# Optimization experiments

Measured on AMD Instinct MI355X. Metric: run time of the kernel, lower is better.

## Reference

```python
import jax, jax.numpy as jnp
import numpy as np

# Dimensions
T, B = 128, 512
NTOK, NINP, NHID = 512, 512, 600
NB, BS, TOPK = 6, 100, 4          # num_blocks, block_size = nhid//num_blocks, update_topk
H, DK, DV, ATT = 4, 64, 85, 340   # input-attention heads, key dim, value dim (H*DV == attention_out)
H2, DK2, DV2 = 4, 32, 32          # communication (step) attention dims


def setup_inputs() -> dict:
    key = jax.random.key(0)
    ks = jax.random.split(key, 16)
    def rn(k, shape, s=0.05):
        return (jax.random.normal(k, shape) * s).astype(jnp.float32)
    return dict(
        input=jax.random.normal(ks[0], (T, B, NTOK), dtype=jnp.float32),
        h0=jnp.zeros((B, NHID), jnp.float32),
        masks=jnp.ones((T, B, 1), jnp.float32),
        enc_W=rn(ks[1], (NTOK, NINP)), enc_b=jnp.zeros((NINP,), jnp.float32),
        Wq_in=rn(ks[2], (BS, H * DK)), Wk_in=rn(ks[3], (NINP, H * DK)), Wv_in=rn(ks[4], (NINP, H * DV)),
        W_ih=rn(ks[5], (NB, ATT, 3 * BS)), W_hh=rn(ks[6], (NB, BS, 3 * BS)),
        b_ih=jnp.zeros((NB, 3 * BS), jnp.float32), b_hh=jnp.zeros((NB, 3 * BS), jnp.float32),
        Wq_c=rn(ks[7], (BS, H2 * DK2)), Wk_c=rn(ks[8], (BS, H2 * DK2)),
        Wv_c=rn(ks[9], (BS, H2 * DV2)), Wo_c=rn(ks[10], (H2 * DV2, BS)),
        dec_W=rn(ks[11], (NHID, NTOK)), dec_b=jnp.zeros((NTOK,), jnp.float32),
    )


def _rim_scan(emb, masks, h0, Wq_in, Wk_in, Wv_in, W_ih, W_hh, b_ih, b_hh,
              Wq_c, Wk_c, Wv_c, Wo_c):
    inv_sdk = 1.0 / np.sqrt(DK).astype(np.float32)
    inv_sdk2 = 1.0 / np.sqrt(DK2).astype(np.float32)

    def step(h, xm):
        xt, mt = xm                      # [B,NINP], [B,1]
        h = h * mt                       # episode-reset gating
        hb = h.reshape(B, NB, BS)
        # --- input attention over {real input, null} slots ---
        slots = jnp.stack([xt, jnp.zeros_like(xt)], axis=1)          # [B,2,NINP]
        k = (slots @ Wk_in).reshape(B, 2, H, DK)
        v = (slots @ Wv_in).reshape(B, 2, H, DV)
        q = (hb @ Wq_in).reshape(B, NB, H, DK)
        att = jax.nn.softmax(jnp.einsum('bnhd,bshd->bnhs', q, k) * inv_sdk, axis=-1)
        act = 1.0 - att[..., 1].mean(-1)                             # [B,NB] attention to real input
        kth = jax.lax.top_k(act, TOPK)[0][:, -1:]
        mask = (act >= kth).astype(h.dtype)                          # [B,NB] top-k block activation
        inp_use = jnp.einsum('bnhs,bshd->bnhd', att, v).reshape(B, NB, ATT)
        # --- block-diagonal GRU update ---
        gi = jnp.einsum('bnd,nde->bne', inp_use, W_ih) + b_ih
        gh = jnp.einsum('bnd,nde->bne', hb, W_hh) + b_hh
        gi_r, gi_z, gi_n = jnp.split(gi, 3, axis=-1)
        gh_r, gh_z, gh_n = jnp.split(gh, 3, axis=-1)
        r = jax.nn.sigmoid(gi_r + gh_r)
        z = jax.nn.sigmoid(gi_z + gh_z)
        n = jnp.tanh(gi_n + r * gh_n)
        hn = (1.0 - z) * n + z * hb
        # --- step (communication) attention across blocks, residual ---
        qc = (hn @ Wq_c).reshape(B, NB, H2, DK2)
        kc = (hn @ Wk_c).reshape(B, NB, H2, DK2)
        vc = (hn @ Wv_c).reshape(B, NB, H2, DV2)
        ac = jax.nn.softmax(jnp.einsum('bnhd,bmhd->bhnm', qc, kc) * inv_sdk2, axis=-1)
        co = jnp.einsum('bhnm,bmhd->bnhd', ac, vc).reshape(B, NB, H2 * DV2) @ Wo_c
        hc = hn + co
        # --- only top-k active blocks are updated ---
        m = mask[..., None]
        hf = (m * hc + (1.0 - m) * hb).reshape(B, NHID)
        return hf, (hf, mask)

    h_last, (hs, bmask) = jax.lax.scan(step, h0, (emb, masks))
    return hs, h_last, bmask


def reference(input, h0, masks, enc_W, enc_b, Wq_in, Wk_in, Wv_in,
              W_ih, W_hh, b_ih, b_hh, Wq_c, Wk_c, Wv_c, Wo_c, dec_W, dec_b):
    emb = input @ enc_W + enc_b                                      # encoder Linear [T,B,NINP]
    hs, h_last, bmask = _rim_scan(emb, masks, h0, Wq_in, Wk_in, Wv_in,
                                  W_ih, W_hh, b_ih, b_hh, Wq_c, Wk_c, Wv_c, Wo_c)
    dec = hs @ dec_W + dec_b                                         # decoder [T,B,NTOK]
    return dec
```

## Files before the change

kernel.cpp:

```cpp
#include <hip/hip_runtime.h>
#include <math.h>

#define T_STEPS 128
#define BATCH   512
#define NTOK    512
#define NINP    512
#define NHID    600
#define NBK     6
#define BS      100
#define HH      4
#define DK      64
#define DV      85
#define ATT     340
#define H2      4
#define DK2     32
#define DV2     32
#define G3      300
#define VN      340
#define KAPN    400
#define CN      740
#define CNP     768
#define UN2     1800
#define UN2P    1920
#define UK0     128
#define KV0     512
#define DECKP   640
#define SW      2

typedef __attribute__((ext_vector_type(8))) short short8;
typedef __attribute__((ext_vector_type(4))) short short4v;
typedef __attribute__((ext_vector_type(4))) float f32x4;

typedef __attribute__((address_space(1))) const unsigned int* g1ptr;
typedef __attribute__((address_space(3))) unsigned int* l3ptr;

__device__ __forceinline__ float sigf(float x) { return 1.f / (1.f + expf(-x)); }
__device__ __forceinline__ unsigned short f2b(float f) {
    unsigned u = __float_as_uint(f);
    unsigned r = (u + 0x7fffu + ((u >> 16) & 1u)) >> 16;
    return (unsigned short)r;
}
__device__ __forceinline__ float b2f(unsigned short u) {
    return __uint_as_float(((unsigned)u) << 16);
}
__device__ __forceinline__ void split3(float x, unsigned short& hi,
                                       unsigned short& mid, unsigned short& lo) {
    hi = f2b(x);
    float r1 = x - b2f(hi);
    mid = f2b(r1);
    lo = f2b(r1 - b2f(mid));
}

struct ZOff { int div; long s1; long s2; };
__device__ __forceinline__ long zoff(ZOff z, int bz) {
    return (long)(bz / z.div) * z.s1 + (long)(bz % z.div) * z.s2;
}

__device__ __forceinline__ void stage_tile(const unsigned short* __restrict__ gbase,
                                           long rowStride, int m0, int k0,
                                           unsigned short* lds, int tid)
{
    const int w = tid >> 6;
#pragma unroll
    for (int q = 0; q < 4; q++) {
        int idx = (q << 8) + tid;
        int r = idx >> 3, ce = (idx & 7) << 3;
        const unsigned short* g = gbase + (long)(m0 + r) * rowStride + k0 + ce;
        unsigned short* l = lds + q * 2048 + w * 512;
        __builtin_amdgcn_global_load_lds((g1ptr)(const void*)g, (l3ptr)(void*)l, 16, 0, 0);
    }
}
__device__ __forceinline__ void stage_tile64(const unsigned short* __restrict__ gbase,
                                             long rowStride, int m0, int k0,
                                             unsigned short* lds, int tid)
{
    const int w = tid >> 6;
#pragma unroll
    for (int q = 0; q < 2; q++) {
        int idx = (q << 8) + tid;
        int r = idx >> 3, ce = (idx & 7) << 3;
        const unsigned short* g = gbase + (long)(m0 + r) * rowStride + k0 + ce;
        unsigned short* l = lds + q * 2048 + w * 512;
        __builtin_amdgcn_global_load_lds((g1ptr)(const void*)g, (l3ptr)(void*)l, 16, 0, 0);
    }
}

__global__ __launch_bounds__(256) void gemm6(
    const unsigned short* __restrict__ A, long aZ, int aZdiv,
    const unsigned short* __restrict__ B, long bZ,
    float* __restrict__ C, long cZ, int ldc, int Nreal,
    const float* __restrict__ bias, int K0)
{
    const int bz = blockIdx.z;
    A += (long)(bz / aZdiv) * aZ;
    B += (long)bz * bZ;
    C += (long)bz * cZ;
    const int LDA = 3 * K0;
    const int m0 = blockIdx.y * 128, n0 = blockIdx.x * 128;
    __shared__ __align__(16) unsigned short As[128 * 64];
    __shared__ __align__(16) unsigned short Bs[128 * 64];
    const int tid = threadIdx.x;
    const int lane = tid & 63;
    const int wid = tid >> 6;
    const int wr = wid >> 1, wc = wid & 1;

    f32x4 acc[4][4];
#pragma unroll
    for (int m = 0; m < 4; m++)
#pragma unroll
        for (int n = 0; n < 4; n++)
#pragma unroll
            for (int v = 0; v < 4; v++) acc[m][n][v] = 0.f;

    const int segA[6] = {0, 0, 1, 0, 2, 1};
    const int segB[6] = {0, 1, 0, 2, 0, 1};
    for (int p = 0; p < 6; p++) {
        const unsigned short* Ap = A + segA[p] * K0;
        const unsigned short* Bp = B + segB[p] * K0;
        for (int k0 = 0; k0 < K0; k0 += 64) {
            __syncthreads();
            stage_tile(Ap, LDA, m0, k0, As, tid);
            stage_tile(Bp, LDA, n0, k0, Bs, tid);
            __syncthreads();
#pragma unroll
            for (int kk = 0; kk < 2; kk++) {
                short8 af[4], bfr[4];
#pragma unroll
                for (int m = 0; m < 4; m++)
                    af[m] = *(const short8*)&As[(wr * 64 + m * 16 + (lane & 15)) * 64 + kk * 32 + (lane >> 4) * 8];
#pragma unroll
                for (int n = 0; n < 4; n++)
                    bfr[n] = *(const short8*)&Bs[(wc * 64 + n * 16 + (lane & 15)) * 64 + kk * 32 + (lane >> 4) * 8];
#pragma unroll
                for (int m = 0; m < 4; m++)
#pragma unroll
                    for (int n = 0; n < 4; n++)
                        acc[m][n] = __builtin_amdgcn_mfma_f32_16x16x32_bf16(af[m], bfr[n], acc[m][n], 0, 0, 0);
            }
        }
    }
#pragma unroll
    for (int m = 0; m < 4; m++) {
        int rbase = m0 + wr * 64 + m * 16 + (lane >> 4) * 4;
#pragma unroll
        for (int n = 0; n < 4; n++) {
            int col = n0 + wc * 64 + n * 16 + (lane & 15);
            if (col < Nreal) {
                float bv = bias ? bias[col] : 0.f;
#pragma unroll
                for (int v = 0; v < 4; v++)
                    C[(long)(rbase + v) * ldc + col] = acc[m][n][v] + bv;
            }
        }
    }
}

__global__ __launch_bounds__(256) void gemm6_kv64(
    const unsigned short* __restrict__ A,
    const unsigned short* __restrict__ B,
    unsigned short* __restrict__ A_U,
    float* __restrict__ Kbuf,
    const float* __restrict__ bias, int K0, int MU)
{
    const int LDA = 3 * K0;
    const int m0 = blockIdx.y * 64, n0 = blockIdx.x * 128;
    __shared__ __align__(16) unsigned short As[64 * 64];
    __shared__ __align__(16) unsigned short Bs[128 * 64];
    const int tid = threadIdx.x;
    const int lane = tid & 63;
    const int w = tid >> 6;

    f32x4 acc[4][2];
#pragma unroll
    for (int m = 0; m < 4; m++)
#pragma unroll
        for (int n = 0; n < 2; n++)
#pragma unroll
            for (int v = 0; v < 4; v++) acc[m][n][v] = 0.f;

    const int segA[6] = {0, 0, 1, 0, 2, 1};
    const int segB[6] = {0, 1, 0, 2, 0, 1};
    for (int p = 0; p < 6; p++) {
        const unsigned short* Ap = A + segA[p] * K0;
        const unsigned short* Bp = B + segB[p] * K0;
        for (int k0 = 0; k0 < K0; k0 += 64) {
            __syncthreads();
            stage_tile64(Ap, LDA, m0, k0, As, tid);
            stage_tile(Bp, LDA, n0, k0, Bs, tid);
            __syncthreads();
#pragma unroll
            for (int kk = 0; kk < 2; kk++) {
                short8 af[4], bfr[2];
#pragma unroll
                for (int m = 0; m < 4; m++)
                    af[m] = *(const short8*)&As[(m * 16 + (lane & 15)) * 64 + kk * 32 + (lane >> 4) * 8];
#pragma unroll
                for (int n = 0; n < 2; n++)
                    bfr[n] = *(const short8*)&Bs[(w * 32 + n * 16 + (lane & 15)) * 64 + kk * 32 + (lane >> 4) * 8];
#pragma unroll
                for (int m = 0; m < 4; m++)
#pragma unroll
                    for (int n = 0; n < 2; n++)
                        acc[m][n] = __builtin_amdgcn_mfma_f32_16x16x32_bf16(af[m], bfr[n], acc[m][n], 0, 0, 0);
            }
        }
    }
#pragma unroll
    for (int m = 0; m < 4; m++) {
        int rbase = m0 + m * 16 + (lane >> 4) * 4;
#pragma unroll
        for (int n = 0; n < 2; n++) {
            int col = n0 + w * 32 + n * 16 + (lane & 15);
            if (col < CN) {
                float bv = bias[col];
                if (col < VN) {
                    int h = col / DV, kk2 = col - h * DV;
#pragma unroll
                    for (int v = 0; v < 4; v++) {
                        float val = acc[m][n][v] + bv;
                        unsigned short hi, mid, lo;
                        split3(val, hi, mid, lo);
                        long base = ((long)h * MU + (rbase + v)) * (3 * UK0) + kk2;
                        A_U[base] = hi;
                        A_U[base + UK0] = mid;
                        A_U[base + 2 * UK0] = lo;
                    }
                } else {
                    int kc = col - VN;
#pragma unroll
                    for (int v = 0; v < 4; v++)
                        Kbuf[(long)(rbase + v) * KAPN + kc] = acc[m][n][v] + bv;
                }
            }
        }
    }
}

__global__ __launch_bounds__(256) void gemm_mfma64(
    const unsigned short* __restrict__ A,
    const unsigned short* __restrict__ B,
    float* __restrict__ C, int ldc,
    const float* __restrict__ bias, int Kp)
{
    const int m0 = blockIdx.y * 64, n0 = blockIdx.x * 128;
    __shared__ __align__(16) unsigned short As[64 * 64];
    __shared__ __align__(16) unsigned short Bs[128 * 64];
    const int tid = threadIdx.x;
    const int lane = tid & 63;
    const int w = tid >> 6;

    f32x4 acc[4][2];
#pragma unroll
    for (int m = 0; m < 4; m++)
#pragma unroll
        for (int n = 0; n < 2; n++)
#pragma unroll
            for (int v = 0; v < 4; v++) acc[m][n][v] = 0.f;

    for (int k0 = 0; k0 < Kp; k0 += 64) {
        __syncthreads();
        stage_tile64(A, Kp, m0, k0, As, tid);
        stage_tile(B, Kp, n0, k0, Bs, tid);
        __syncthreads();
#pragma unroll
        for (int kk = 0; kk < 2; kk++) {
            short8 af[4], bfr[2];
#pragma unroll
            for (int m = 0; m < 4; m++)
                af[m] = *(const short8*)&As[(m * 16 + (lane & 15)) * 64 + kk * 32 + (lane >> 4) * 8];
#pragma unroll
            for (int n = 0; n < 2; n++)
                bfr[n] = *(const short8*)&Bs[(w * 32 + n * 16 + (lane & 15)) * 64 + kk * 32 + (lane >> 4) * 8];
#pragma unroll
            for (int m = 0; m < 4; m++)
#pragma unroll
                for (int n = 0; n < 2; n++)
                    acc[m][n] = __builtin_amdgcn_mfma_f32_16x16x32_bf16(af[m], bfr[n], acc[m][n], 0, 0, 0);
        }
    }
#pragma unroll
    for (int m = 0; m < 4; m++) {
        int rbase = m0 + m * 16 + (lane >> 4) * 4;
#pragma unroll
        for (int n = 0; n < 2; n++) {
            int col = n0 + w * 32 + n * 16 + (lane & 15);
            float bv = bias ? bias[col] : 0.f;
#pragma unroll
            for (int v = 0; v < 4; v++)
                C[(long)(rbase + v) * ldc + col] = acc[m][n][v] + bv;
        }
    }
}

__global__ __launch_bounds__(256) void sgemm(
    const float* __restrict__ A, ZOff za, int lda,
    const float* __restrict__ B, ZOff zb, int ldb,
    float* __restrict__ C, ZOff zc, int ldc,
    int M, int N, int K)
{
    const int bz = blockIdx.z;
    A += zoff(za, bz);
    B += zoff(zb, bz);
    C += zoff(zc, bz);
    const int m0 = blockIdx.y * 128, n0 = blockIdx.x * 64;
    __shared__ float As[16][132];
    __shared__ float Bs[16][68];
    const int tid = threadIdx.x;
    const int tm = tid >> 4, tn = tid & 15;
    const int ar = tid >> 1, ak = (tid & 1) * 8;
    const int bk = tid >> 4, bn = (tid & 15) * 4;

    float acc[8][4];
#pragma unroll
    for (int i = 0; i < 8; i++)
#pragma unroll
        for (int j = 0; j < 4; j++) acc[i][j] = 0.f;

    for (int k0 = 0; k0 < K; k0 += 16) {
        float av[8], bv[4];
#pragma unroll
        for (int j = 0; j < 8; j++) {
            int gk = k0 + ak + j;
            av[j] = (gk < K) ? A[(long)(m0 + ar) * lda + gk] : 0.f;
        }
#pragma unroll
        for (int j = 0; j < 4; j++) {
            int gk = k0 + bk, gn = n0 + bn + j;
            bv[j] = (gk < K && gn < N) ? B[(long)gk * ldb + gn] : 0.f;
        }
        __syncthreads();
#pragma unroll
        for (int j = 0; j < 8; j++) As[ak + j][ar] = av[j];
#pragma unroll
        for (int j = 0; j < 4; j++) Bs[bk][bn + j] = bv[j];
        __syncthreads();
#pragma unroll
        for (int kk = 0; kk < 16; kk++) {
            float a[8], b[4];
#pragma unroll
            for (int i = 0; i < 8; i++) a[i] = As[kk][tm * 8 + i];
#pragma unroll
            for (int j = 0; j < 4; j++) b[j] = Bs[kk][tn * 4 + j];
#pragma unroll
            for (int i = 0; i < 8; i++)
#pragma unroll
                for (int j = 0; j < 4; j++)
                    acc[i][j] += a[i] * b[j];
        }
    }
#pragma unroll
    for (int i = 0; i < 8; i++) {
        int gm = m0 + tm * 8 + i;
#pragma unroll
        for (int j = 0; j < 4; j++) {
            int gn = n0 + tn * 4 + j;
            if (gn < N) C[(long)gm * ldc + gn] = acc[i][j];
        }
    }
}

__global__ __launch_bounds__(256) void prep_wqt(const float* __restrict__ Wq_in,
                                                float* __restrict__ WqT)
{
    int idx = blockIdx.x * 256 + threadIdx.x;
    if (idx >= HH * DK * BS) return;
    int h = idx / (DK * BS), r = idx - h * DK * BS, d = r / BS, w = r - d * BS;
    WqT[idx] = Wq_in[w * (HH * DK) + h * DK + d];
}

__global__ __launch_bounds__(256) void prep_whh4(const float* __restrict__ W_hh,
                                                 float* __restrict__ Whh4)
{
    int idx = blockIdx.x * 256 + threadIdx.x;
    if (idx >= NBK * BS * G3) return;
    int n = idx / (BS * G3), r = idx - n * (BS * G3);
    int d = r / G3, e = r - d * G3;
    int g = e / BS, w = e - g * BS;
    Whh4[(((long)n * BS + d) * BS + w) * 4 + g] = W_hh[idx];
}

__global__ __launch_bounds__(256) void bias_k(const float* __restrict__ enc_b,
                                              const float* __restrict__ Wk,
                                              float* __restrict__ kbf)
{
    int j = threadIdx.x;
    if (j >= HH * DK) return;
    float acc = 0.f;
    for (int d = 0; d < NINP; d++) acc += enc_b[d] * Wk[d * (HH * DK) + j];
    kbf[j] = acc;
}

__global__ __launch_bounds__(256) void bias_c_kernel(const float* __restrict__ enc_b,
                                                     const float* __restrict__ Wv,
                                                     const float* __restrict__ kbf,
                                                     const float* __restrict__ WqT,
                                                     float* __restrict__ bias_c)
{
    int j = blockIdx.x * 256 + threadIdx.x;
    if (j >= CNP) return;
    float acc = 0.f;
    if (j < VN) {
        for (int d = 0; d < NINP; d++) acc += enc_b[d] * Wv[d * (HH * DV) + j];
    } else if (j < CN) {
        int r = j - VN;
        int h = r / BS, w = r - h * BS;
        for (int d = 0; d < DK; d++)
            acc += kbf[h * DK + d] * WqT[(h * DK + d) * BS + w];
    }
    bias_c[j] = acc;
}

__global__ __launch_bounds__(256) void cvt_dec(const float* __restrict__ dec_W,
                                               unsigned short* __restrict__ dst)
{
    int idx = blockIdx.x * 256 + threadIdx.x;
    if (idx >= NTOK * DECKP) return;
    int n = idx / DECKP, k = idx - n * DECKP;
    dst[idx] = f2b(k < NHID ? dec_W[k * NTOK + n] : 0.f);
}

__global__ __launch_bounds__(256) void cvt_split_ew(const float* __restrict__ EWfull,
                                                    unsigned short* __restrict__ dst)
{
    int idx = blockIdx.x * 256 + threadIdx.x;
    if (idx >= CNP * NTOK) return;
    int n = idx / NTOK, k = idx - n * NTOK;
    float x = (n < CN) ? EWfull[(long)k * CNP + n] : 0.f;
    unsigned short hi, mid, lo;
    split3(x, hi, mid, lo);
    long base = (long)n * (3 * KV0) + k;
    dst[base] = hi;
    dst[base + KV0] = mid;
    dst[base + 2 * KV0] = lo;
}

__global__ __launch_bounds__(256) void cvt_split_bu2(const float* __restrict__ W_ih,
                                                     unsigned short* __restrict__ dst)
{
    int idx = blockIdx.x * 256 + threadIdx.x;
    if (idx >= HH * UN2P * UK0) return;
    int h = idx / (UN2P * UK0), r = idx - h * (UN2P * UK0);
    int j = r / UK0, kk = r - j * UK0;
    float x = 0.f;
    if (kk < DV && j < UN2) {
        int n = j / G3, e = j - n * G3;
        x = W_ih[((long)n * ATT + h * DV + kk) * G3 + e];
    }
    unsigned short hi, mid, lo;
    split3(x, hi, mid, lo);
    long base = ((long)h * UN2P + j) * (3 * UK0) + kk;
    dst[base] = hi;
    dst[base + UK0] = mid;
    dst[base + 2 * UK0] = lo;
}

__global__ __launch_bounds__(256) void cvt_split_in(const float* __restrict__ src,
                                                    unsigned short* __restrict__ dst, long rows)
{
    long total = rows * (NTOK / 4);
    long i = (long)blockIdx.x * 256 + threadIdx.x;
    long stride = (long)gridDim.x * 256;
    for (; i < total; i += stride) {
        long row = i / (NTOK / 4);
        int k4 = (int)(i - row * (NTOK / 4)) * 4;
        f32x4 x = *(const f32x4*)&src[row * NTOK + k4];
        short4v hi, mid, lo;
#pragma unroll
        for (int j = 0; j < 4; j++) {
            unsigned short h, m, l;
            split3(x[j], h, m, l);
            hi[j] = (short)h; mid[j] = (short)m; lo[j] = (short)l;
        }
        long base = row * (3 * KV0) + k4;
        *(short4v*)&dst[base] = hi;
        *(short4v*)&dst[base + KV0] = mid;
        *(short4v*)&dst[base + 2 * KV0] = lo;
    }
}

__global__ __launch_bounds__(1024) void step_fused(
    const float* __restrict__ h_prev,
    const float* __restrict__ masks_t,
    const float* __restrict__ Kbuf,
    const float* __restrict__ U,
    const float* __restrict__ b_ih, const float* __restrict__ b_hh,
    const float* __restrict__ Whh4,
    const float* __restrict__ Wq_c, const float* __restrict__ Wk_c,
    const float* __restrict__ Wv_c, const float* __restrict__ Wo_c,
    float* __restrict__ h_out,
    unsigned short* __restrict__ A_dec,
    int s_step, int MU)
{
    const int b0 = blockIdx.x * SW, tid = threadIdx.x;
    __shared__ __align__(16) float hbT[NHID][SW];
    __shared__ __align__(16) float hnT[NHID][SW];
    __shared__ __align__(16) float kp[SW][KAPN];
    __shared__ __align__(16) float qcb[SW][768], kcb[SW][768], vcb[SW][768];
    __shared__ __align__(16) float coT[NBK * 128][SW];
    __shared__ float part[SW * 96];
    __shared__ float att[SW][24], mk[SW][NBK];
    __shared__ float lg[SW][144];

    const long rowd0 = (long)s_step * BATCH + b0;
    const int n2 = (tid < 600) ? tid / 100 : 0;
    const int w2 = (tid < 600) ? tid - n2 * 100 : 0;

    float uraw[HH][3][SW];
    if (tid < 600) {
#pragma unroll
        for (int h = 0; h < HH; h++) {
            const float* Uh = U + ((long)h * MU + rowd0) * UN2 + n2 * G3;
#pragma unroll
            for (int s = 0; s < SW; s++)
#pragma unroll
                for (int g = 0; g < 3; g++)
                    uraw[h][g][s] = Uh[(long)s * UN2 + g * BS + w2];
        }
    }

    for (int i = tid; i < SW * NHID; i += 1024) {
        int s = i / NHID, j = i - s * NHID;
        hbT[j][s] = h_prev[(long)(b0 + s) * NHID + j] * masks_t[b0 + s];
    }
    for (int i = tid; i < SW * KAPN; i += 1024) {
        int s = i / KAPN, j = i - s * KAPN;
        kp[s][j] = Kbuf[(rowd0 + s) * KAPN + j];
    }
    __syncthreads();
    if (tid < SW * 96) {
        int g = tid >> 2, q = tid & 3;
        int s = g / 24, r = g - s * 24;
        int n = r >> 2, h = r & 3;
        float acc = 0.f;
        int w0 = q * 25;
        for (int w = w0; w < w0 + 25; w++) acc += hbT[n * BS + w][s] * kp[s][h * BS + w];
        part[tid] = acc;
    }
    __syncthreads();
    if (tid < SW * 24) {
        int s = tid / 24, r = tid - s * 24;
        float l = part[tid * 4] + part[tid * 4 + 1] + part[tid * 4 + 2] + part[tid * 4 + 3];
        att[s][r] = sigf(l * 0.125f);
    }
    __syncthreads();
    if (tid < SW) {
        float a[NBK], av[NBK];
        for (int n = 0; n < NBK; n++) {
            av[n] = 0.25f * (att[tid][n * 4] + att[tid][n * 4 + 1] + att[tid][n * 4 + 2] + att[tid][n * 4 + 3]);
            a[n] = av[n];
        }
        for (int i = 0; i < 4; i++) {
            int mx = i;
            for (int j = i + 1; j < NBK; j++) if (a[j] > a[mx]) mx = j;
            float t = a[i]; a[i] = a[mx]; a[mx] = t;
        }
        float kth = a[3];
        for (int n = 0; n < NBK; n++) mk[tid][n] = (av[n] >= kth) ? 1.f : 0.f;
    }

    if (tid < 600) {
        float gi[3][SW], gh[3][SW];
#pragma unroll
        for (int g = 0; g < 3; g++) {
            float bi = b_ih[n2 * G3 + g * BS + w2];
            float bh = b_hh[n2 * G3 + g * BS + w2];
#pragma unroll
            for (int s = 0; s < SW; s++) { gi[g][s] = bi; gh[g][s] = bh; }
        }
#pragma unroll
        for (int h = 0; h < HH; h++)
#pragma unroll
            for (int s = 0; s < SW; s++) {
                float a = att[s][n2 * 4 + h];
#pragma unroll
                for (int g = 0; g < 3; g++)
                    gi[g][s] += a * uraw[h][g][s];
            }
        const f32x4* Wn4 = ((const f32x4*)Whh4) + (long)n2 * BS * BS + w2;
#pragma unroll 10
        for (int d = 0; d < BS; d++) {
            f32x4 wv = Wn4[(long)d * BS];
            float2 hv = *(const float2*)&hbT[n2 * BS + d][0];
            gh[0][0] += wv[0] * hv.x; gh[0][1] += wv[0] * hv.y;
            gh[1][0] += wv[1] * hv.x; gh[1][1] += wv[1] * hv.y;
            gh[2][0] += wv[2] * hv.x; gh[2][1] += wv[2] * hv.y;
        }
        float2 hnv;
        {
            float rr0 = sigf(gi[0][0] + gh[0][0]);
            float zz0 = sigf(gi[1][0] + gh[1][0]);
            float ng0 = tanhf(gi[2][0] + rr0 * gh[2][0]);
            hnv.x = (1.f - zz0) * ng0 + zz0 * hbT[n2 * BS + w2][0];
            float rr1 = sigf(gi[0][1] + gh[0][1]);
            float zz1 = sigf(gi[1][1] + gh[1][1]);
            float ng1 = tanhf(gi[2][1] + rr1 * gh[2][1]);
            hnv.y = (1.f - zz1) * ng1 + zz1 * hbT[n2 * BS + w2][1];
        }
        *(float2*)&hnT[n2 * BS + w2][0] = hnv;
    }
    __syncthreads();

    if (tid < 768) {
        const int mat = tid >> 8, r = tid & 255, ng = r >> 7, c = r & 127;
        const float* W = (mat == 0) ? Wq_c : ((mat == 1) ? Wk_c : Wv_c);
        float acc[3][SW];
#pragma unroll
        for (int j = 0; j < 3; j++)
#pragma unroll
            for (int s = 0; s < SW; s++) acc[j][s] = 0.f;
#pragma unroll 10
        for (int d = 0; d < BS; d++) {
            float wv = W[d * 128 + c];
#pragma unroll
            for (int j = 0; j < 3; j++) {
                float2 hv = *(const float2*)&hnT[(ng * 3 + j) * BS + d][0];
                acc[j][0] += wv * hv.x;
                acc[j][1] += wv * hv.y;
            }
        }
        float (*dst)[768] = (mat == 0) ? qcb : ((mat == 1) ? kcb : vcb);
#pragma unroll
        for (int j = 0; j < 3; j++)
#pragma unroll
            for (int s = 0; s < SW; s++)
                dst[s][(ng * 3 + j) * 128 + c] = acc[j][s];
    }
    __syncthreads();

    if (tid < SW * 144) {
        int s = tid / 144, r = tid - s * 144;
        int h = r / 36, r2 = r - h * 36, n = r2 / NBK, m = r2 - n * NBK;
        float sv = 0.f;
#pragma unroll
        for (int e4 = 0; e4 < 8; e4++) {
            f32x4 qv = *(const f32x4*)&qcb[s][n * 128 + h * 32 + e4 * 4];
            f32x4 kv = *(const f32x4*)&kcb[s][m * 128 + h * 32 + e4 * 4];
            sv += qv[0] * kv[0] + qv[1] * kv[1] + qv[2] * kv[2] + qv[3] * kv[3];
        }
        lg[s][r] = sv * 0.17677669529663687f;
    }
    __syncthreads();
    if (tid < SW * 24) {
        int s = tid / 24, r = tid - s * 24;
        float* row = &lg[s][r * NBK];
        float mx = row[0];
        for (int m = 1; m < NBK; m++) mx = fmaxf(mx, row[m]);
        float sv = 0.f;
        for (int m = 0; m < NBK; m++) { row[m] = expf(row[m] - mx); sv += row[m]; }
        float inv = 1.f / sv;
        for (int m = 0; m < NBK; m++) row[m] *= inv;
    }
    __syncthreads();
    for (int idx = tid; idx < SW * 768; idx += 1024) {
        int s = idx / 768, r = idx - s * 768;
        int n = r >> 7, d = r & 127, h = d >> 5;
        float a = 0.f;
#pragma unroll
        for (int m = 0; m < NBK; m++) a += lg[s][h * 36 + n * NBK + m] * vcb[s][m * 128 + d];
        coT[r][s] = a;
    }
    __syncthreads();

    if (tid < 600) {
        float a0 = 0.f, a1 = 0.f;
#pragma unroll 8
        for (int d = 0; d < 128; d++) {
            float wv = Wo_c[d * BS + w2];
            float2 cv = *(const float2*)&coT[n2 * 128 + d][0];
            a0 += wv * cv.x;
            a1 += wv * cv.y;
        }
        float2 res;
        float hc0 = hnT[n2 * BS + w2][0] + a0;
        float hc1 = hnT[n2 * BS + w2][1] + a1;
        res.x = (mk[0][n2] > 0.5f) ? hc0 : hbT[n2 * BS + w2][0];
        res.y = (mk[1][n2] > 0.5f) ? hc1 : hbT[n2 * BS + w2][1];
        *(float2*)&hbT[n2 * BS + w2][0] = res;
    }
    __syncthreads();
    for (int i = tid; i < SW * NHID; i += 1024) {
        int s = i / NHID, j = i - s * NHID;
        h_out[(long)(b0 + s) * NHID + j] = hbT[j][s];
    }
    for (int i = tid; i < SW * DECKP; i += 1024) {
        int s = i / DECKP, col = i - s * DECKP;
        A_dec[(rowd0 + s) * DECKP + col] = f2b(col < NHID ? hbT[col][s] : 0.f);
    }
}

extern "C" void kernel_launch(void* const* d_in, const int* in_sizes, int n_in,
                              void* d_out, int out_size, void* d_ws, size_t ws_size,
                              hipStream_t stream)
{
    const float* input = (const float*)d_in[0];
    const float* h0    = (const float*)d_in[1];
    const float* masks = (const float*)d_in[2];
    const float* enc_W = (const float*)d_in[3];
    const float* enc_b = (const float*)d_in[4];
    const float* Wq_in = (const float*)d_in[5];
    const float* Wk_in = (const float*)d_in[6];
    const float* Wv_in = (const float*)d_in[7];
    const float* W_ih  = (const float*)d_in[8];
    const float* W_hh  = (const float*)d_in[9];
    const float* b_ih  = (const float*)d_in[10];
    const float* b_hh  = (const float*)d_in[11];
    const float* Wq_c  = (const float*)d_in[12];
    const float* Wk_c  = (const float*)d_in[13];
    const float* Wv_c  = (const float*)d_in[14];
    const float* Wo_c  = (const float*)d_in[15];
    const float* dec_W = (const float*)d_in[16];
    const float* dec_b = (const float*)d_in[17];
    float* out = (float*)d_out;

    const size_t AL = 256;
    auto pad = [&](size_t x) { return (x + AL - 1) & ~(AL - 1); };
    size_t fixedB = pad((size_t)NTOK * CNP * 4)
                  + pad((size_t)NTOK * 256 * 4)
                  + pad((size_t)HH * DK * BS * 4)
                  + pad((size_t)256 * 4)
                  + pad((size_t)CNP * 4)
                  + pad((size_t)NBK * BS * BS * 4 * 4)
                  + pad((size_t)CNP * 3 * KV0 * 2)
                  + pad((size_t)HH * UN2P * 3 * UK0 * 2)
                  + pad((size_t)NTOK * DECKP * 2)
                  + 2 * pad((size_t)BATCH * NHID * 4);
    auto perC = [&](int C) {
        size_t MU = (size_t)C * BATCH;
        return pad(MU * 3 * KV0 * 2)
             + pad(MU * KAPN * 4)
             + pad((size_t)HH * MU * 3 * UK0 * 2)
             + pad((size_t)HH * MU * UN2 * 4)
             + pad(MU * DECKP * 2);
    };
    int C = 8;
    while (C > 1 && fixedB + perC(C) > ws_size) C >>= 1;
    const int MU = C * BATCH;
    const int NCH = T_STEPS / C;

    char* p = (char*)d_ws;
    auto alloc = [&](size_t bytes) { char* r = p; p += pad(bytes); return r; };
    float*          EWfull = (float*)alloc((size_t)NTOK * CNP * 4);
    float*          EWk    = (float*)alloc((size_t)NTOK * 256 * 4);
    float*          WqT    = (float*)alloc((size_t)HH * DK * BS * 4);
    float*          kbf    = (float*)alloc((size_t)256 * 4);
    float*          bias_c = (float*)alloc((size_t)CNP * 4);
    float*          Whh4   = (float*)alloc((size_t)NBK * BS * BS * 4 * 4);
    unsigned short* B_vkap = (unsigned short*)alloc((size_t)CNP * 3 * KV0 * 2);
    unsigned short* B_U    = (unsigned short*)alloc((size_t)HH * UN2P * 3 * UK0 * 2);
    unsigned short* B_dec  = (unsigned short*)alloc((size_t)NTOK * DECKP * 2);
    float*          hA     = (float*)alloc((size_t)BATCH * NHID * 4);
    float*          hB     = (float*)alloc((size_t)BATCH * NHID * 4);
    unsigned short* A_in   = (unsigned short*)alloc((size_t)MU * 3 * KV0 * 2);
    float*          Kbuf   = (float*)alloc((size_t)MU * KAPN * 4);
    unsigned short* A_U    = (unsigned short*)alloc((size_t)HH * MU * 3 * UK0 * 2);
    float*          Ubuf   = (float*)alloc((size_t)HH * MU * UN2 * 4);
    unsigned short* A_dec  = (unsigned short*)alloc((size_t)MU * DECKP * 2);

    dim3 blk(256);
    ZOff z0 = {1, 0, 0};

    sgemm<<<dim3(6, 4, 1), blk, 0, stream>>>(
        enc_W, z0, NINP, Wv_in, z0, HH * DV, EWfull, z0, CNP, NTOK, VN, NINP);
    sgemm<<<dim3(4, 4, 1), blk, 0, stream>>>(
        enc_W, z0, NINP, Wk_in, z0, HH * DK, EWk, z0, 256, NTOK, HH * DK, NINP);
    prep_wqt<<<dim3((HH * DK * BS + 255) / 256), blk, 0, stream>>>(Wq_in, WqT);
    prep_whh4<<<dim3((NBK * BS * G3 + 255) / 256), blk, 0, stream>>>(W_hh, Whh4);
    sgemm<<<dim3(2, 4, HH), blk, 0, stream>>>(
        EWk, ZOff{1, DK, 0}, 256, WqT, ZOff{1, (long)DK * BS, 0}, BS,
        EWfull + VN, ZOff{1, BS, 0}, CNP, NTOK, BS, DK);
    bias_k<<<dim3(1), blk, 0, stream>>>(enc_b, Wk_in, kbf);
    bias_c_kernel<<<dim3(3), blk, 0, stream>>>(enc_b, Wv_in, kbf, WqT, bias_c);
    cvt_split_ew<<<dim3((CNP * NTOK + 255) / 256), blk, 0, stream>>>(EWfull, B_vkap);
    cvt_split_bu2<<<dim3((HH * UN2P * UK0 + 255) / 256), blk, 0, stream>>>(W_ih, B_U);
    cvt_dec<<<dim3((NTOK * DECKP + 255) / 256), blk, 0, stream>>>(dec_W, B_dec);

    const float* hp = h0;
    float* hbufs[2] = { hA, hB };
    int t = 0;
    for (int c = 0; c < NCH; c++) {
        cvt_split_in<<<dim3(2048), blk, 0, stream>>>(
            input + (size_t)c * MU * NTOK, A_in, MU);
        gemm6_kv64<<<dim3(CNP / 128, MU / 64, 1), blk, 0, stream>>>(
            A_in, B_vkap, A_U, Kbuf, bias_c, KV0, MU);
        gemm6<<<dim3(UN2P / 128, MU / 128, HH), blk, 0, stream>>>(
            A_U, (long)MU * 3 * UK0, 1, B_U, (long)UN2P * 3 * UK0,
            Ubuf, (long)MU * UN2, UN2, UN2, nullptr, UK0);
        for (int s = 0; s < C; s++, t++) {
            float* hout = hbufs[t & 1];
            step_fused<<<dim3(BATCH / SW), dim3(1024), 0, stream>>>(
                hp, masks + (size_t)t * BATCH, Kbuf, Ubuf, b_ih, b_hh, Whh4,
                Wq_c, Wk_c, Wv_c, Wo_c, hout, A_dec, s, MU);
            hp = hout;
        }
        gemm_mfma64<<<dim3(NTOK / 128, MU / 64, 1), blk, 0, stream>>>(
            A_dec, B_dec, out + (size_t)c * MU * NTOK, NTOK, dec_b, DECKP);
    }
}
```

Before: 5.991 ms.

## Process one batch row per block with 512 threads in step kernel

The per-timestep fused RIM kernel now handles one batch element per workgroup with 512 threads, instead of two elements per workgroup with 1024 threads. The grid doubles to 512 blocks, and each thread covers one or two hidden units and projection columns. This spreads the sequential step across more workgroups and CUs and lowers per-block LDS use. In exchange, every weight row (W_hh, Wq/k/v_c, Wo_c) is now read once per batch element rather than shared across two, which doubles weight traffic from cache.

Result: slower. 7.497 ms (+25.1%).

```diff
diff --git a/kernel.cpp b/kernel.cpp
--- a/kernel.cpp
+++ b/kernel.cpp
@@ -25,7 +25,6 @@
 #define UK0     128
 #define KV0     512
 #define DECKP   640
-#define SW      2
 
 typedef __attribute__((ext_vector_type(8))) short short8;
 typedef __attribute__((ext_vector_type(4))) short short4v;
@@ -478,7 +477,7 @@
     }
 }
 
-__global__ __launch_bounds__(1024) void step_fused(
+__global__ __launch_bounds__(512) void step_fused(
     const float* __restrict__ h_prev,
     const float* __restrict__ masks_t,
     const float* __restrict__ Kbuf,
@@ -491,62 +490,68 @@
     unsigned short* __restrict__ A_dec,
     int s_step, int MU)
 {
-    const int b0 = blockIdx.x * SW, tid = threadIdx.x;
-    __shared__ __align__(16) float hbT[NHID][SW];
-    __shared__ __align__(16) float hnT[NHID][SW];
-    __shared__ __align__(16) float kp[SW][KAPN];
-    __shared__ __align__(16) float qcb[SW][768], kcb[SW][768], vcb[SW][768];
-    __shared__ __align__(16) float coT[NBK * 128][SW];
-    __shared__ float part[SW * 96];
-    __shared__ float att[SW][24], mk[SW][NBK];
-    __shared__ float lg[SW][144];
-
-    const long rowd0 = (long)s_step * BATCH + b0;
-    const int n2 = (tid < 600) ? tid / 100 : 0;
-    const int w2 = (tid < 600) ? tid - n2 * 100 : 0;
-
-    float uraw[HH][3][SW];
-    if (tid < 600) {
+    const int b = blockIdx.x, tid = threadIdx.x;
+    __shared__ __align__(16) float hb[NHID];
+    __shared__ __align__(16) float hn[NHID];
+    __shared__ __align__(16) float kp[KAPN];
+    __shared__ __align__(16) float qcb[768], kcb[768], vcb[768];
+    __shared__ __align__(16) float co[768];
+    __shared__ float part[96];
+    __shared__ float att[24], mk[NBK];
+    __shared__ float lg[144];
+
+    const long rowd = (long)s_step * BATCH + b;
+    const int oA = tid;
+    const int nA = oA / 100, wA = oA - nA * 100;
+    const bool hasB = tid < 88;
+    const int oB = tid + 512;
+    const int nB = oB / 100, wB = oB - nB * 100;
+
+    float urA[HH][3], urB[HH][3];
+    {
+        const float* Ub = U + rowd * UN2;
 #pragma unroll
         for (int h = 0; h < HH; h++) {
-            const float* Uh = U + ((long)h * MU + rowd0) * UN2 + n2 * G3;
-#pragma unroll
-            for (int s = 0; s < SW; s++)
+            const float* Uh = Ub + (long)h * MU * UN2;
+#pragma unroll
+            for (int g = 0; g < 3; g++)
+                urA[h][g] = Uh[nA * G3 + g * BS + wA];
+        }
+        if (hasB) {
+#pragma unroll
+            for (int h = 0; h < HH; h++) {
+                const float* Uh = Ub + (long)h * MU * UN2;
 #pragma unroll
                 for (int g = 0; g < 3; g++)
-                    uraw[h][g][s] = Uh[(long)s * UN2 + g * BS + w2];
-        }
-    }
-
-    for (int i = tid; i < SW * NHID; i += 1024) {
-        int s = i / NHID, j = i - s * NHID;
-        hbT[j][s] = h_prev[(long)(b0 + s) * NHID + j] * masks_t[b0 + s];
-    }
-    for (int i = tid; i < SW * KAPN; i += 1024) {
-        int s = i / KAPN, j = i - s * KAPN;
-        kp[s][j] = Kbuf[(rowd0 + s) * KAPN + j];
+                    urB[h][g] = Uh[nB * G3 + g * BS + wB];
+            }
+        }
+    }
+
+    const float mt = masks_t[b];
+    for (int i = tid; i < NHID; i += 512) hb[i] = h_prev[(long)b * NHID + i] * mt;
+    if (tid >= 512 - KAPN || true) {
+        for (int i = tid; i < KAPN; i += 512) kp[i] = Kbuf[rowd * KAPN + i];
     }
     __syncthreads();
-    if (tid < SW * 96) {
-        int g = tid >> 2, q = tid & 3;
-        int s = g / 24, r = g - s * 24;
+    if (tid < 96) {
+        int r = tid >> 2, q = tid & 3;
         int n = r >> 2, h = r & 3;
         float acc = 0.f;
         int w0 = q * 25;
-        for (int w = w0; w < w0 + 25; w++) acc += hbT[n * BS + w][s] * kp[s][h * BS + w];
+        for (int w = w0; w < w0 + 25; w++) acc += hb[n * BS + w] * kp[h * BS + w];
         part[tid] = acc;
     }
     __syncthreads();
-    if (tid < SW * 24) {
-        int s = tid / 24, r = tid - s * 24;
+    if (tid < 24) {
         float l = part[tid * 4] + part[tid * 4 + 1] + part[tid * 4 + 2] + part[tid * 4 + 3];
-        att[s][r] = sigf(l * 0.125f);
+        att[tid] = sigf(l * 0.125f);
     }
     __syncthreads();
-    if (tid < SW) {
+    if (tid == 0) {
         float a[NBK], av[NBK];
         for (int n = 0; n < NBK; n++) {
-            av[n] = 0.25f * (att[tid][n * 4] + att[tid][n * 4 + 1] + att[tid][n * 4 + 2] + att[tid][n * 4 + 3]);
+            av[n] = 0.25f * (att[n * 4] + att[n * 4 + 1] + att[n * 4 + 2] + att[n * 4 + 3]);
             a[n] = av[n];
         }
         for (int i = 0; i < 4; i++) {
@@ -555,94 +560,116 @@
             float t = a[i]; a[i] = a[mx]; a[mx] = t;
         }
         float kth = a[3];
-        for (int n = 0; n < NBK; n++) mk[tid][n] = (av[n] >= kth) ? 1.f : 0.f;
-    }
-
-    if (tid < 600) {
-        float gi[3][SW], gh[3][SW];
-#pragma unroll
-        for (int g = 0; g < 3; g++) {
-            float bi = b_ih[n2 * G3 + g * BS + w2];
-            float bh = b_hh[n2 * G3 + g * BS + w2];
-#pragma unroll
-            for (int s = 0; s < SW; s++) { gi[g][s] = bi; gh[g][s] = bh; }
-        }
-#pragma unroll
-        for (int h = 0; h < HH; h++)
-#pragma unroll
-            for (int s = 0; s < SW; s++) {
-                float a = att[s][n2 * 4 + h];
-#pragma unroll
-                for (int g = 0; g < 3; g++)
-                    gi[g][s] += a * uraw[h][g][s];
-            }
-        const f32x4* Wn4 = ((const f32x4*)Whh4) + (long)n2 * BS * BS + w2;
+        for (int n = 0; n < NBK; n++) mk[n] = (av[n] >= kth) ? 1.f : 0.f;
+    }
+
+    {
+        float gi0 = b_ih[nA * G3 + wA], gi1 = b_ih[nA * G3 + BS + wA], gi2 = b_ih[nA * G3 + 2 * BS + wA];
+        float gh0 = b_hh[nA * G3 + wA], gh1 = b_hh[nA * G3 + BS + wA], gh2 = b_hh[nA * G3 + 2 * BS + wA];
+#pragma unroll
+        for (int h = 0; h < HH; h++) {
+            float a = att[nA * 4 + h];
+            gi0 += a * urA[h][0];
+            gi1 += a * urA[h][1];
+            gi2 += a * urA[h][2];
+        }
+        float gj0 = 0.f, gj1 = 0.f, gj2 = 0.f;
+        if (hasB) {
+            gj0 = b_hh[nB * G3 + wB]; gj1 = b_hh[nB * G3 + BS + wB]; gj2 = b_hh[nB * G3 + 2 * BS + wB];
+        }
+        const f32x4* WA = ((const f32x4*)Whh4) + (long)nA * BS * BS + wA;
+        const f32x4* WB = ((const f32x4*)Whh4) + (long)nB * BS * BS + wB;
 #pragma unroll 10
         for (int d = 0; d < BS; d++) {
-            f32x4 wv = Wn4[(long)d * BS];
-            float2 hv = *(const float2*)&hbT[n2 * BS + d][0];
-            gh[0][0] += wv[0] * hv.x; gh[0][1] += wv[0] * hv.y;
-            gh[1][0] += wv[1] * hv.x; gh[1][1] += wv[1] * hv.y;
-            gh[2][0] += wv[2] * hv.x; gh[2][1] += wv[2] * hv.y;
-        }
-        float2 hnv;
+            f32x4 wv = WA[(long)d * BS];
+            float hv = hb[nA * BS + d];
+            gh0 += wv[0] * hv;
+            gh1 += wv[1] * hv;
+            gh2 += wv[2] * hv;
+        }
+        if (hasB) {
+#pragma unroll 10
+            for (int d = 0; d < BS; d++) {
+                f32x4 wv = WB[(long)d * BS];
+                float hv = hb[nB * BS + d];
+                gj0 += wv[0] * hv;
+                gj1 += wv[1] * hv;
+                gj2 += wv[2] * hv;
+            }
+        }
         {
-            float rr0 = sigf(gi[0][0] + gh[0][0]);
-            float zz0 = sigf(gi[1][0] + gh[1][0]);
-            float ng0 = tanhf(gi[2][0] + rr0 * gh[2][0]);
-            hnv.x = (1.f - zz0) * ng0 + zz0 * hbT[n2 * BS + w2][0];
-            float rr1 = sigf(gi[0][1] + gh[0][1]);
-            float zz1 = sigf(gi[1][1] + gh[1][1]);
-            float ng1 = tanhf(gi[2][1] + rr1 * gh[2][1]);
-            hnv.y = (1.f - zz1) * ng1 + zz1 * hbT[n2 * BS + w2][1];
-        }
-        *(float2*)&hnT[n2 * BS + w2][0] = hnv;
+            float rr = sigf(gi0 + gh0);
+            float zz = sigf(gi1 + gh1);
+            float ng = tanhf(gi2 + rr * gh2);
+            hn[oA] = (1.f - zz) * ng + zz * hb[oA];
+        }
+        if (hasB) {
+            float fi0 = b_ih[nB * G3 + wB], fi1 = b_ih[nB * G3 + BS + wB], fi2 = b_ih[nB * G3 + 2 * BS + wB];
+#pragma unroll
+            for (int h = 0; h < HH; h++) {
+                float a = att[nB * 4 + h];
+                fi0 += a * urB[h][0];
+                fi1 += a * urB[h][1];
+                fi2 += a * urB[h][2];
+            }
+            float rr = sigf(fi0 + gj0);
+            float zz = sigf(fi1 + gj1);
+            float ng = tanhf(fi2 + rr * gj2);
+            hn[oB] = (1.f - zz) * ng + zz * hb[oB];
+        }
     }
     __syncthreads();
 
-    if (tid < 768) {
-        const int mat = tid >> 8, r = tid & 255, ng = r >> 7, c = r & 127;
-        const float* W = (mat == 0) ? Wq_c : ((mat == 1) ? Wk_c : Wv_c);
-        float acc[3][SW];
-#pragma unroll
-        for (int j = 0; j < 3; j++)
-#pragma unroll
-            for (int s = 0; s < SW; s++) acc[j][s] = 0.f;
+    {
+        const int matA = tid >> 8, ngA = (tid >> 7) & 1, cA = tid & 127;
+        const float* Wa = (matA == 0) ? Wq_c : Wk_c;
+        float accA3[3] = {0.f, 0.f, 0.f};
+        const bool hasB3 = tid < 256;
+        const int ngB = tid >> 7, cB = tid & 127;
+        float accB3[3] = {0.f, 0.f, 0.f};
 #pragma unroll 10
         for (int d = 0; d < BS; d++) {
-            float wv = W[d * 128 + c];
-#pragma unroll
-            for (int j = 0; j < 3; j++) {
-                float2 hv = *(const float2*)&hnT[(ng * 3 + j) * BS + d][0];
-                acc[j][0] += wv * hv.x;
-                acc[j][1] += wv * hv.y;
+            float wv = Wa[d * 128 + cA];
+#pragma unroll
+            for (int j = 0; j < 3; j++)
+                accA3[j] += wv * hn[(ngA * 3 + j) * BS + d];
+        }
+        if (hasB3) {
+#pragma unroll 10
+            for (int d = 0; d < BS; d++) {
+                float wv = Wv_c[d * 128 + cB];
+#pragma unroll
+                for (int j = 0; j < 3; j++)
+                    accB3[j] += wv * hn[(ngB * 3 + j) * BS + d];
             }
         }
-        float (*dst)[768] = (mat == 0) ? qcb : ((mat == 1) ? kcb : vcb);
+        float* dstA = (matA == 0) ? qcb : kcb;
 #pragma unroll
         for (int j = 0; j < 3; j++)
-#pragma unroll
-            for (int s = 0; s < SW; s++)
-                dst[s][(ng * 3 + j) * 128 + c] = acc[j][s];
+            dstA[(ngA * 3 + j) * 128 + cA] = accA3[j];
+        if (hasB3) {
+#pragma unroll
+            for (int j = 0; j < 3; j++)
+                vcb[(ngB * 3 + j) * 128 + cB] = accB3[j];
+        }
     }
     __syncthreads();
 
-    if (tid < SW * 144) {
-        int s = tid / 144, r = tid - s * 144;
-        int h = r / 36, r2 = r - h * 36, n = r2 / NBK, m = r2 - n * NBK;
+    if (tid < 144) {
+        int h = tid / 36, r2 = tid - h * 36, n = r2 / NBK, m = r2 - n * NBK;
         float sv = 0.f;
 #pragma unroll
         for (int e4 = 0; e4 < 8; e4++) {
-            f32x4 qv = *(const f32x4*)&qcb[s][n * 128 + h * 32 + e4 * 4];
-            f32x4 kv = *(const f32x4*)&kcb[s][m * 128 + h * 32 + e4 * 4];
+            f32x4 qv = *(const f32x4*)&qcb[n * 128 + h * 32 + e4 * 4];
+            f32x4 kv = *(const f32x4*)&kcb[m * 128 + h * 32 + e4 * 4];
             sv += qv[0] * kv[0] + qv[1] * kv[1] + qv[2] * kv[2] + qv[3] * kv[3];
         }
-        lg[s][r] = sv * 0.17677669529663687f;
+        lg[tid] = sv * 0.17677669529663687f;
     }
     __syncthreads();
-    if (tid < SW * 24) {
-        int s = tid / 24, r = tid - s * 24;
-        float* row = &lg[s][r * NBK];
+    if (tid < 24) {
+        int h = tid / NBK, n = tid - h * NBK;
+        float* row = &lg[h * 36 + n * NBK];
         float mx = row[0];
         for (int m = 1; m < NBK; m++) mx = fmaxf(mx, row[m]);
         float sv = 0.f;
@@ -651,41 +678,54 @@
         for (int m = 0; m < NBK; m++) row[m] *= inv;
     }
     __syncthreads();
-    for (int idx = tid; idx < SW * 768; idx += 1024) {
-        int s = idx / 768, r = idx - s * 768;
+    {
+        int r = tid;
         int n = r >> 7, d = r & 127, h = d >> 5;
         float a = 0.f;
 #pragma unroll
-        for (int m = 0; m < NBK; m++) a += lg[s][h * 36 + n * NBK + m] * vcb[s][m * 128 + d];
-        coT[r][s] = a;
+        for (int m = 0; m < NBK; m++) a += lg[h * 36 + n * NBK + m] * vcb[m * 128 + d];
+        co[r] = a;
+        if (tid < 256) {
+            int r2 = tid + 512;
+            int n2 = r2 >> 7, d2 = r2 & 127, h2 = d2 >> 5;
+            float a2 = 0.f;
+#pragma unroll
+            for (int m = 0; m < NBK; m++) a2 += lg[h2 * 36 + n2 * NBK + m] * vcb[m * 128 + d2];
+            co[r2] = a2;
+        }
     }
     __syncthreads();
 
-    if (tid < 600) {
+    {
         float a0 = 0.f, a1 = 0.f;
 #pragma unroll 8
         for (int d = 0; d < 128; d++) {
-            float wv = Wo_c[d * BS + w2];
-            float2 cv = *(const float2*)&coT[n2 * 128 + d][0];
-            a0 += wv * cv.x;
-            a1 += wv * cv.y;
-        }
-        float2 res;
-        float hc0 = hnT[n2 * BS + w2][0] + a0;
-        float hc1 = hnT[n2 * BS + w2][1] + a1;
-        res.x = (mk[0][n2] > 0.5f) ? hc0 : hbT[n2 * BS + w2][0];
-        res.y = (mk[1][n2] > 0.5f) ? hc1 : hbT[n2 * BS + w2][1];
-        *(float2*)&hbT[n2 * BS + w2][0] = res;
+            float cvA = co[nA * 128 + d];
+            a0 += Wo_c[d * BS + wA] * cvA;
+        }
+        if (hasB) {
+#pragma unroll 8
+            for (int d = 0; d < 128; d++) {
+                float cvB = co[nB * 128 + d];
+                a1 += Wo_c[d * BS + wB] * cvB;
+            }
+        }
+        float hcA = hn[oA] + a0;
+        float resA = (mk[nA] > 0.5f) ? hcA : hb[oA];
+        float resB = 0.f;
+        if (hasB) {
+            float hcB = hn[oB] + a1;
+            resB = (mk[nB] > 0.5f) ? hcB : hb[oB];
+        }
+        __syncthreads();
+        hb[oA] = resA;
+        if (hasB) hb[oB] = resB;
     }
     __syncthreads();
-    for (int i = tid; i < SW * NHID; i += 1024) {
-        int s = i / NHID, j = i - s * NHID;
-        h_out[(long)(b0 + s) * NHID + j] = hbT[j][s];
-    }
-    for (int i = tid; i < SW * DECKP; i += 1024) {
-        int s = i / DECKP, col = i - s * DECKP;
-        A_dec[(rowd0 + s) * DECKP + col] = f2b(col < NHID ? hbT[col][s] : 0.f);
-    }
+    for (int i = tid; i < NHID; i += 512)
+        h_out[(long)b * NHID + i] = hb[i];
+    for (int i = tid; i < DECKP; i += 512)
+        A_dec[rowd * DECKP + i] = f2b(i < NHID ? hb[i] : 0.f);
 }
 
 extern "C" void kernel_launch(void* const* d_in, const int* in_sizes, int n_in,
@@ -787,7 +827,7 @@
             Ubuf, (long)MU * UN2, UN2, UN2, nullptr, UK0);
         for (int s = 0; s < C; s++, t++) {
             float* hout = hbufs[t & 1];
-            step_fused<<<dim3(BATCH / SW), dim3(1024), 0, stream>>>(
+            step_fused<<<dim3(BATCH), dim3(512), 0, stream>>>(
                 hp, masks + (size_t)t * BATCH, Kbuf, Ubuf, b_ih, b_hh, Whh4,
                 Wq_c, Wk_c, Wv_c, Wo_c, hout, A_dec, s, MU);
             hp = hout;
```

## Fuse input bf16x3 split into KV GEMM and reuse segment tiles across products

Applied to the files above, without the earlier changes.

Removes the separate cvt_split_in pass and its workspace buffer. The KV GEMM now loads fp32 input directly, splits each value into hi/mid/lo bf16 in registers and writes all three segments to LDS. Both split-precision GEMMs now stage all three segments once per k-tile and run the six cross products from LDS, instead of restaging a tile for every product. The U GEMM also moves from 128x128 to 64x128 tiles to give more blocks. The cost is about three times the LDS per block (72KB), which may lower occupancy.

Measured after the change: 5.419 ms. 1.11x faster.

```diff
diff --git a/kernel.cpp b/kernel.cpp
--- a/kernel.cpp
+++ b/kernel.cpp
@@ -85,87 +85,86 @@
     }
 }
 
-__global__ __launch_bounds__(256) void gemm6(
-    const unsigned short* __restrict__ A, long aZ, int aZdiv,
+__global__ __launch_bounds__(256) void gemm6_useg(
+    const unsigned short* __restrict__ A, long aZ,
     const unsigned short* __restrict__ B, long bZ,
-    float* __restrict__ C, long cZ, int ldc, int Nreal,
-    const float* __restrict__ bias, int K0)
+    float* __restrict__ C, long cZ, int ldc, int Nreal, int K0)
 {
     const int bz = blockIdx.z;
-    A += (long)(bz / aZdiv) * aZ;
+    A += (long)bz * aZ;
     B += (long)bz * bZ;
     C += (long)bz * cZ;
     const int LDA = 3 * K0;
-    const int m0 = blockIdx.y * 128, n0 = blockIdx.x * 128;
-    __shared__ __align__(16) unsigned short As[128 * 64];
-    __shared__ __align__(16) unsigned short Bs[128 * 64];
+    const int m0 = blockIdx.y * 64, n0 = blockIdx.x * 128;
+    __shared__ __align__(16) unsigned short As3[3][64 * 64];
+    __shared__ __align__(16) unsigned short Bs3[3][128 * 64];
     const int tid = threadIdx.x;
     const int lane = tid & 63;
-    const int wid = tid >> 6;
-    const int wr = wid >> 1, wc = wid & 1;
-
-    f32x4 acc[4][4];
+    const int w = tid >> 6;
+
+    f32x4 acc[4][2];
 #pragma unroll
     for (int m = 0; m < 4; m++)
 #pragma unroll
-        for (int n = 0; n < 4; n++)
+        for (int n = 0; n < 2; n++)
 #pragma unroll
             for (int v = 0; v < 4; v++) acc[m][n][v] = 0.f;
 
     const int segA[6] = {0, 0, 1, 0, 2, 1};
     const int segB[6] = {0, 1, 0, 2, 0, 1};
-    for (int p = 0; p < 6; p++) {
-        const unsigned short* Ap = A + segA[p] * K0;
-        const unsigned short* Bp = B + segB[p] * K0;
-        for (int k0 = 0; k0 < K0; k0 += 64) {
-            __syncthreads();
-            stage_tile(Ap, LDA, m0, k0, As, tid);
-            stage_tile(Bp, LDA, n0, k0, Bs, tid);
-            __syncthreads();
+    for (int k0 = 0; k0 < K0; k0 += 64) {
+        __syncthreads();
+#pragma unroll
+        for (int s = 0; s < 3; s++) stage_tile64(A + s * K0, LDA, m0, k0, As3[s], tid);
+#pragma unroll
+        for (int s = 0; s < 3; s++) stage_tile(B + s * K0, LDA, n0, k0, Bs3[s], tid);
+        __syncthreads();
+#pragma unroll
+        for (int p = 0; p < 6; p++) {
+            const unsigned short* Asl = As3[segA[p]];
+            const unsigned short* Bsl = Bs3[segB[p]];
 #pragma unroll
             for (int kk = 0; kk < 2; kk++) {
-                short8 af[4], bfr[4];
+                short8 af[4], bfr[2];
 #pragma unroll
                 for (int m = 0; m < 4; m++)
-                    af[m] = *(const short8*)&As[(wr * 64 + m * 16 + (lane & 15)) * 64 + kk * 32 + (lane >> 4) * 8];
-#pragma unroll
-                for (int n = 0; n < 4; n++)
-                    bfr[n] = *(const short8*)&Bs[(wc * 64 + n * 16 + (lane & 15)) * 64 + kk * 32 + (lane >> 4) * 8];
+                    af[m] = *(const short8*)&Asl[(m * 16 + (lane & 15)) * 64 + kk * 32 + (lane >> 4) * 8];
+#pragma unroll
+                for (int n = 0; n < 2; n++)
+                    bfr[n] = *(const short8*)&Bsl[(w * 32 + n * 16 + (lane & 15)) * 64 + kk * 32 + (lane >> 4) * 8];
 #pragma unroll
                 for (int m = 0; m < 4; m++)
 #pragma unroll
-                    for (int n = 0; n < 4; n++)
+                    for (int n = 0; n < 2; n++)
                         acc[m][n] = __builtin_amdgcn_mfma_f32_16x16x32_bf16(af[m], bfr[n], acc[m][n], 0, 0, 0);
             }
         }
     }
 #pragma unroll
     for (int m = 0; m < 4; m++) {
-        int rbase = m0 + wr * 64 + m * 16 + (lane >> 4) * 4;
-#pragma unroll
-        for (int n = 0; n < 4; n++) {
-            int col = n0 + wc * 64 + n * 16 + (lane & 15);
+        int rbase = m0 + m * 16 + (lane >> 4) * 4;
+#pragma unroll
+        for (int n = 0; n < 2; n++) {
+            int col = n0 + w * 32 + n * 16 + (lane & 15);
             if (col < Nreal) {
-                float bv = bias ? bias[col] : 0.f;
 #pragma unroll
                 for (int v = 0; v < 4; v++)
-                    C[(long)(rbase + v) * ldc + col] = acc[m][n][v] + bv;
+                    C[(long)(rbase + v) * ldc + col] = acc[m][n][v];
             }
         }
     }
 }
 
-__global__ __launch_bounds__(256) void gemm6_kv64(
-    const unsigned short* __restrict__ A,
+__global__ __launch_bounds__(256) void gemm6_kvseg(
+    const float* __restrict__ X,
     const unsigned short* __restrict__ B,
     unsigned short* __restrict__ A_U,
     float* __restrict__ Kbuf,
-    const float* __restrict__ bias, int K0, int MU)
-{
-    const int LDA = 3 * K0;
+    const float* __restrict__ bias, int MU)
+{
     const int m0 = blockIdx.y * 64, n0 = blockIdx.x * 128;
-    __shared__ __align__(16) unsigned short As[64 * 64];
-    __shared__ __align__(16) unsigned short Bs[128 * 64];
+    __shared__ __align__(16) unsigned short As3[3][64 * 64];
+    __shared__ __align__(16) unsigned short Bs3[3][128 * 64];
     const int tid = threadIdx.x;
     const int lane = tid & 63;
     const int w = tid >> 6;
@@ -180,23 +179,46 @@
 
     const int segA[6] = {0, 0, 1, 0, 2, 1};
     const int segB[6] = {0, 1, 0, 2, 0, 1};
-    for (int p = 0; p < 6; p++) {
-        const unsigned short* Ap = A + segA[p] * K0;
-        const unsigned short* Bp = B + segB[p] * K0;
-        for (int k0 = 0; k0 < K0; k0 += 64) {
-            __syncthreads();
-            stage_tile64(Ap, LDA, m0, k0, As, tid);
-            stage_tile(Bp, LDA, n0, k0, Bs, tid);
-            __syncthreads();
+    for (int k0 = 0; k0 < KV0; k0 += 64) {
+        f32x4 xv[4];
+#pragma unroll
+        for (int q = 0; q < 4; q++) {
+            int idx = (q << 8) + tid;
+            int r = idx >> 4, c4 = (idx & 15) << 2;
+            xv[q] = *(const f32x4*)&X[(long)(m0 + r) * KV0 + k0 + c4];
+        }
+        __syncthreads();
+#pragma unroll
+        for (int s = 0; s < 3; s++) stage_tile(B + s * KV0, 3 * KV0, n0, k0, Bs3[s], tid);
+#pragma unroll
+        for (int q = 0; q < 4; q++) {
+            int idx = (q << 8) + tid;
+            int r = idx >> 4, c4 = (idx & 15) << 2;
+            short4v hs, ms, ls;
+#pragma unroll
+            for (int j = 0; j < 4; j++) {
+                unsigned short h, m, l;
+                split3(xv[q][j], h, m, l);
+                hs[j] = (short)h; ms[j] = (short)m; ls[j] = (short)l;
+            }
+            *(short4v*)&As3[0][r * 64 + c4] = hs;
+            *(short4v*)&As3[1][r * 64 + c4] = ms;
+            *(short4v*)&As3[2][r * 64 + c4] = ls;
+        }
+        __syncthreads();
+#pragma unroll
+        for (int p = 0; p < 6; p++) {
+            const unsigned short* Asl = As3[segA[p]];
+            const unsigned short* Bsl = Bs3[segB[p]];
 #pragma unroll
             for (int kk = 0; kk < 2; kk++) {
                 short8 af[4], bfr[2];
 #pragma unroll
                 for (int m = 0; m < 4; m++)
-                    af[m] = *(const short8*)&As[(m * 16 + (lane & 15)) * 64 + kk * 32 + (lane >> 4) * 8];
+                    af[m] = *(const short8*)&Asl[(m * 16 + (lane & 15)) * 64 + kk * 32 + (lane >> 4) * 8];
 #pragma unroll
                 for (int n = 0; n < 2; n++)
-                    bfr[n] = *(const short8*)&Bs[(w * 32 + n * 16 + (lane & 15)) * 64 + kk * 32 + (lane >> 4) * 8];
+                    bfr[n] = *(const short8*)&Bsl[(w * 32 + n * 16 + (lane & 15)) * 64 + kk * 32 + (lane >> 4) * 8];
 #pragma unroll
                 for (int m = 0; m < 4; m++)
 #pragma unroll
@@ -452,30 +474,6 @@
     dst[base] = hi;
     dst[base + UK0] = mid;
     dst[base + 2 * UK0] = lo;
-}
-
-__global__ __launch_bounds__(256) void cvt_split_in(const float* __restrict__ src,
-                                                    unsigned short* __restrict__ dst, long rows)
-{
-    long total = rows * (NTOK / 4);
-    long i = (long)blockIdx.x * 256 + threadIdx.x;
-    long stride = (long)gridDim.x * 256;
-    for (; i < total; i += stride) {
-        long row = i / (NTOK / 4);
-        int k4 = (int)(i - row * (NTOK / 4)) * 4;
-        f32x4 x = *(const f32x4*)&src[row * NTOK + k4];
-        short4v hi, mid, lo;
-#pragma unroll
-        for (int j = 0; j < 4; j++) {
-            unsigned short h, m, l;
-            split3(x[j], h, m, l);
-            hi[j] = (short)h; mid[j] = (short)m; lo[j] = (short)l;
-        }
-        long base = row * (3 * KV0) + k4;
-        *(short4v*)&dst[base] = hi;
-        *(short4v*)&dst[base + KV0] = mid;
-        *(short4v*)&dst[base + 2 * KV0] = lo;
-    }
 }
 
 __global__ __launch_bounds__(1024) void step_fused(
@@ -726,8 +724,7 @@
                   + 2 * pad((size_t)BATCH * NHID * 4);
     auto perC = [&](int C) {
         size_t MU = (size_t)C * BATCH;
-        return pad(MU * 3 * KV0 * 2)
-             + pad(MU * KAPN * 4)
+        return pad(MU * KAPN * 4)
              + pad((size_t)HH * MU * 3 * UK0 * 2)
              + pad((size_t)HH * MU * UN2 * 4)
              + pad(MU * DECKP * 2);
@@ -750,7 +747,6 @@
     unsigned short* B_dec  = (unsigned short*)alloc((size_t)NTOK * DECKP * 2);
     float*          hA     = (float*)alloc((size_t)BATCH * NHID * 4);
     float*          hB     = (float*)alloc((size_t)BATCH * NHID * 4);
-    unsigned short* A_in   = (unsigned short*)alloc((size_t)MU * 3 * KV0 * 2);
     float*          Kbuf   = (float*)alloc((size_t)MU * KAPN * 4);
     unsigned short* A_U    = (unsigned short*)alloc((size_t)HH * MU * 3 * UK0 * 2);
     float*          Ubuf   = (float*)alloc((size_t)HH * MU * UN2 * 4);
@@ -778,13 +774,11 @@
     float* hbufs[2] = { hA, hB };
     int t = 0;
     for (int c = 0; c < NCH; c++) {
-        cvt_split_in<<<dim3(2048), blk, 0, stream>>>(
-            input + (size_t)c * MU * NTOK, A_in, MU);
-        gemm6_kv64<<<dim3(CNP / 128, MU / 64, 1), blk, 0, stream>>>(
-            A_in, B_vkap, A_U, Kbuf, bias_c, KV0, MU);
-        gemm6<<<dim3(UN2P / 128, MU / 128, HH), blk, 0, stream>>>(
-            A_U, (long)MU * 3 * UK0, 1, B_U, (long)UN2P * 3 * UK0,
-            Ubuf, (long)MU * UN2, UN2, UN2, nullptr, UK0);
+        gemm6_kvseg<<<dim3(CNP / 128, MU / 64, 1), blk, 0, stream>>>(
+            input + (size_t)c * MU * NTOK, B_vkap, A_U, Kbuf, bias_c, MU);
+        gemm6_useg<<<dim3(UN2P / 128, MU / 64, HH), blk, 0, stream>>>(
+            A_U, (long)MU * 3 * UK0, B_U, (long)UN2P * 3 * UK0,
+            Ubuf, (long)MU * UN2, UN2, UN2, UK0);
         for (int s = 0; s < C; s++, t++) {
             float* hout = hbufs[t & 1];
             step_fused<<<dim3(BATCH / SW), dim3(1024), 0, stream>>>(
```
